# Performance work log

Measured on AMD Instinct MI355X. Metric: run time of the kernel, lower is better.

The kernel has to match this reference:

```python
import jax, jax.numpy as jnp
import numpy as np

N, L, D = 512, 40, 128      # batch, peptide length, embedding dim
O, K, MHC = 256, 9, 34      # out_channels, kernel_size, mhc_len
STRIDE = 1


def setup_inputs() -> dict:
    key = jax.random.key(0)
    k1, k2, k3 = jax.random.split(key, 3)
    peptide_x = jax.random.normal(k1, (N, L, D), dtype=jnp.float32)
    mhc_x = jax.random.normal(k2, (N, MHC, D), dtype=jnp.float32)
    weight = jax.random.normal(k3, (O, K, MHC), dtype=jnp.float32) * 0.02  # truncated_normal std=0.02 approx
    bias = jnp.zeros((O,), dtype=jnp.float32)
    return {"peptide_x": peptide_x, "mhc_x": mhc_x, "weight": weight, "bias": bias}


def reference(peptide_x, mhc_x, weight, bias):
    # Per-sample dynamic kernel generation: [n, O, d, K]
    kernel = jax.nn.relu(jnp.einsum('nld,okl->nodk', mhc_x, weight))
    k = weight.shape[1]
    T = (peptide_x.shape[1] - k) // STRIDE + 1  # conv1d output length
    # Sliding windows of the peptide: [n, T, K, d]
    idx = jnp.arange(T)[:, None] * STRIDE + jnp.arange(k)[None, :]
    win = peptide_x[:, idx, :]
    # Grouped (groups=batch) conv1d as a batched contraction: [n, O, T]
    out = jnp.einsum('ntkd,nodk->not', win, kernel) + bias[None, :, None]
    return out
```

## Files before the change

kernel.cpp:

```cpp
#include <hip/hip_runtime.h>
#include <hip/hip_bf16.h>

typedef unsigned short u16;
typedef unsigned int u32;
typedef __bf16 bf16x8 __attribute__((ext_vector_type(8)));
typedef float f32x4 __attribute__((ext_vector_type(4)));
typedef unsigned int u32x4 __attribute__((ext_vector_type(4)));
typedef unsigned int u32x2 __attribute__((ext_vector_type(2)));

#define NN 512
#define LL 40
#define DD 128
#define OO 256
#define KK 9
#define MHCL 34
#define TT 32
#define OC 32
#define OCPG 4
#define PSTR 136
#define MSTR 72
#define KSTR 136
#define LPAD 64
#define WPADL 64

#define PEPT_U16 (LL * PSTR)
#define KERN_U16 (32 * KSTR)

__device__ __forceinline__ u16 f2bf(float x) {
    unsigned int u = __builtin_bit_cast(unsigned int, x);
    u = (u + 0x7FFFu + ((u >> 16) & 1u)) >> 16;
    return (u16)u;
}
__device__ __forceinline__ u32 pk2(float a, float b) {
    __hip_bfloat162 h = __float22bfloat162_rn(make_float2(a, b));
    u32 r;
    __builtin_memcpy(&r, &h, 4);
    return r;
}
__device__ __forceinline__ bf16x8 lds_read8(const u16* p) {
    u32x4 r;
    __builtin_memcpy(&r, __builtin_assume_aligned(p, 16), 16);
    return __builtin_bit_cast(bf16x8, r);
}
__device__ __forceinline__ f32x4 mfma16(bf16x8 a, bf16x8 b, f32x4 c) {
    return __builtin_amdgcn_mfma_f32_16x16x32_bf16(a, b, c, 0, 0, 0);
}

__global__ void w_convert(const float* __restrict__ wgt, u32* __restrict__ wp) {
    int i = blockIdx.x * 256 + threadIdx.x;
    if (i >= OO * KK * (WPADL / 2)) return;
    int o = i / (KK * (WPADL / 2));
    int r = i - o * (KK * (WPADL / 2));
    int k = r >> 5;
    int lp = (r & 31) << 1;
    const float* src = wgt + ((size_t)o * KK + k) * MHCL;
    float a = (lp     < MHCL) ? src[lp]     : 0.f;
    float b = (lp + 1 < MHCL) ? src[lp + 1] : 0.f;
    wp[i] = pk2(a, b);
}

template<bool PRE>
__global__ __launch_bounds__(512, 4)
void iconv_kernel(const float* __restrict__ pept,
                  const float* __restrict__ mhc,
                  const float* __restrict__ wgt,
                  const u16* __restrict__ wp,
                  const float* __restrict__ bias,
                  float* __restrict__ out)
{
    __shared__ __align__(16) u16 s_mem[PEPT_U16 + 4 * KERN_U16];

    const int tid  = threadIdx.x;
    const int wave = tid >> 6;
    const int grp  = wave >> 2;
    const int wl   = wave & 3;
    const int lane = tid & 63;
    const int quad = lane >> 4;
    const int l16  = lane & 15;

    const int n = blockIdx.x;

    u16* const s_pept = s_mem;
    u16* const kb0    = s_mem + PEPT_U16 + grp * (2 * KERN_U16);

    auto loadW = [&](int o_base, int k, bf16x8 wF[2][2]) {
        if (PRE) {
            #pragma unroll
            for (int mt = 0; mt < 2; ++mt) {
                const u16* wr = wp + ((size_t)(o_base + mt * 16 + l16) * KK + k) * WPADL;
                u32x4 r0, r1;
                __builtin_memcpy(&r0, __builtin_assume_aligned(wr + quad * 8, 16), 16);
                __builtin_memcpy(&r1, __builtin_assume_aligned(wr + 32 + quad * 8, 16), 16);
                wF[mt][0] = __builtin_bit_cast(bf16x8, r0);
                wF[mt][1] = __builtin_bit_cast(bf16x8, r1);
            }
        } else {
            #pragma unroll
            for (int mt = 0; mt < 2; ++mt) {
                const float* wrow = wgt + ((size_t)(o_base + mt * 16 + l16) * KK + k) * MHCL;
                float w8[8];
                __builtin_memcpy(w8, __builtin_assume_aligned(wrow + quad * 8, 8), 32);
                u16 h0[8];
                #pragma unroll
                for (int j = 0; j < 8; ++j) h0[j] = f2bf(w8[j]);
                __builtin_memcpy(&wF[mt][0], h0, 16);
                u16 h1[8] = {0,0,0,0,0,0,0,0};
                if (quad == 0) { h1[0] = f2bf(wrow[32]); h1[1] = f2bf(wrow[33]); }
                __builtin_memcpy(&wF[mt][1], h1, 16);
            }
        }
    };

    bf16x8 wFh[2][2];
    loadW((grp * OCPG) * OC, 0, wFh);

    {
        const float* mg = mhc + (size_t)n * MHCL * DD;
        #pragma unroll 1
        for (int i = tid; i < DD * (LPAD / 8); i += 512) {
            int g = i >> 7, d = i & 127;
            u32x4 hh;
            #pragma unroll
            for (int jj = 0; jj < 4; ++jj) {
                int l = g * 8 + jj * 2;
                float a = (l     < MHCL) ? mg[(size_t)l * DD + d]       : 0.f;
                float b = (l + 1 < MHCL) ? mg[(size_t)(l + 1) * DD + d] : 0.f;
                hh[jj] = pk2(a, b);
            }
            __builtin_memcpy(__builtin_assume_aligned(&s_mem[d * MSTR + g * 8], 16), &hh, 16);
        }
    }
    __syncthreads();

    bf16x8 aF[2][2];
    #pragma unroll
    for (int ntl = 0; ntl < 2; ++ntl) {
        const int d = (wl * 2 + ntl) * 16 + l16;
        aF[ntl][0] = lds_read8(&s_mem[d * MSTR + quad * 8]);
        aF[ntl][1] = lds_read8(&s_mem[d * MSTR + 32 + quad * 8]);
    }
    __syncthreads();

    {
        const float* pg = pept + (size_t)n * LL * DD;
        #pragma unroll 1
        for (int i = tid; i < (LL * DD) / 4; i += 512) {
            int row = i >> 5, c4 = (i & 31) << 2;
            f32x4 v;
            __builtin_memcpy(&v, __builtin_assume_aligned(pg + row * DD + c4, 16), 16);
            u32x2 h = { pk2(v[0], v[1]), pk2(v[2], v[3]) };
            __builtin_memcpy(__builtin_assume_aligned(&s_pept[row * PSTR + c4], 8), &h, 8);
        }
    }
    __syncthreads();

    auto stage1 = [&](const bf16x8 wF[2][2], int buf) {
        u16* const kbw = kb0 + buf * KERN_U16;
        #pragma unroll
        for (int ntl = 0; ntl < 2; ++ntl) {
            const int nt = wl * 2 + ntl;
            f32x4 c0 = {0.f,0.f,0.f,0.f}, c1 = c0;
            #pragma unroll
            for (int ki = 0; ki < 2; ++ki) {
                c0 = mfma16(aF[ntl][ki], wF[0][ki], c0);
                c1 = mfma16(aF[ntl][ki], wF[1][ki], c1);
            }
            u32x2 p0 = { pk2(fmaxf(c0[0], 0.f), fmaxf(c0[1], 0.f)),
                         pk2(fmaxf(c0[2], 0.f), fmaxf(c0[3], 0.f)) };
            u32x2 p1 = { pk2(fmaxf(c1[0], 0.f), fmaxf(c1[1], 0.f)),
                         pk2(fmaxf(c1[2], 0.f), fmaxf(c1[3], 0.f)) };
            __builtin_memcpy(__builtin_assume_aligned(&kbw[l16 * KSTR + nt * 16 + quad * 4], 8), &p0, 8);
            __builtin_memcpy(__builtin_assume_aligned(&kbw[(16 + l16) * KSTR + nt * 16 + quad * 4], 8), &p1, 8);
        }
    };

    const int off = wl * 32 + quad * 8;

    #pragma unroll 1
    for (int oci = 0; oci < OCPG; ++oci) {
        const int o_base = (grp * OCPG + oci) * OC;
        f32x4 acc00 = {0.f,0.f,0.f,0.f}, acc01 = acc00, acc10 = acc00, acc11 = acc00;

        bf16x8 wCur[2][2];
        loadW(o_base, 1, wCur);
        stage1(wFh, 0);

        #pragma unroll
        for (int k = 0; k < KK; ++k) {
            const u16* kbr = kb0 + (k & 1) * KERN_U16;
            bf16x8 bk0 = lds_read8(&kbr[l16 * KSTR + off]);
            bf16x8 bk1 = lds_read8(&kbr[(16 + l16) * KSTR + off]);
            bf16x8 ap0 = lds_read8(&s_pept[(k + l16) * PSTR + off]);
            bf16x8 ap1 = lds_read8(&s_pept[(k + 16 + l16) * PSTR + off]);
            bf16x8 wNext[2][2];
            if (k + 2 <= KK - 1) loadW(o_base, k + 2, wNext);
            if (k + 1 <= KK - 1) stage1(wCur, (k + 1) & 1);
            acc00 = mfma16(ap0, bk0, acc00);
            acc01 = mfma16(ap0, bk1, acc01);
            acc10 = mfma16(ap1, bk0, acc10);
            acc11 = mfma16(ap1, bk1, acc11);
            if (k + 2 <= KK - 1) {
                #pragma unroll
                for (int a = 0; a < 2; ++a)
                    #pragma unroll
                    for (int b = 0; b < 2; ++b) wCur[a][b] = wNext[a][b];
            }
        }

        if (oci + 1 < OCPG) loadW((grp * OCPG + oci + 1) * OC, 0, wFh);

        __syncthreads();
        float* red = (float*)kb0;
        if (wl < 2) {
            float* rw = red + wl * (TT * 33);
            #pragma unroll
            for (int r = 0; r < 4; ++r) {
                rw[(quad * 4 + r) * 33 + l16]           = acc00[r];
                rw[(quad * 4 + r) * 33 + 16 + l16]      = acc01[r];
                rw[(16 + quad * 4 + r) * 33 + l16]      = acc10[r];
                rw[(16 + quad * 4 + r) * 33 + 16 + l16] = acc11[r];
            }
        }
        __syncthreads();
        if (wl >= 2) {
            float* rw = red + (wl - 2) * (TT * 33);
            #pragma unroll
            for (int r = 0; r < 4; ++r) {
                rw[(quad * 4 + r) * 33 + l16]           += acc00[r];
                rw[(quad * 4 + r) * 33 + 16 + l16]      += acc01[r];
                rw[(16 + quad * 4 + r) * 33 + l16]      += acc10[r];
                rw[(16 + quad * 4 + r) * 33 + 16 + l16] += acc11[r];
            }
        }
        __syncthreads();

        {
            const int lt = tid & 255;
            const int o  = lt >> 3;
            const int t0 = (lt & 7) * 4;
            const float bv = bias[o_base + o];
            f32x4 res;
            #pragma unroll
            for (int j = 0; j < 4; ++j) {
                int idx = (t0 + j) * 33 + o;
                res[j] = red[idx] + red[TT * 33 + idx] + bv;
            }
            float* op = out + ((size_t)n * OO + o_base + o) * TT + t0;
            __builtin_memcpy(__builtin_assume_aligned(op, 16), &res, 16);
        }
        __syncthreads();
    }
}

extern "C" void kernel_launch(void* const* d_in, const int* in_sizes, int n_in,
                              void* d_out, int out_size, void* d_ws, size_t ws_size,
                              hipStream_t stream) {
    const float* pept = (const float*)d_in[0];
    const float* mhc  = (const float*)d_in[1];
    const float* wgt  = (const float*)d_in[2];
    const float* bias = (const float*)d_in[3];
    float* out = (float*)d_out;

    const size_t w_bytes = (size_t)OO * KK * WPADL * sizeof(u16);
    if (ws_size >= w_bytes) {
        w_convert<<<dim3((OO * KK * (WPADL / 2) + 255) / 256), dim3(256), 0, stream>>>(wgt, (u32*)d_ws);
        iconv_kernel<true><<<dim3(NN), dim3(512), 0, stream>>>(pept, mhc, wgt, (const u16*)d_ws, bias, out);
    } else {
        iconv_kernel<false><<<dim3(NN), dim3(512), 0, stream>>>(pept, mhc, wgt, nullptr, bias, out);
    }
}
```

Measured before the change: 144.2 us.

## Process two output-channel chunks per pass, sharing peptide fragments and barriers

Each wave group now handles two 32-channel chunks (A and B) per outer iteration instead of one, so it makes 2 passes rather than 4. Within a pass, the peptide window fragments read from LDS are reused for both chunks' MFMAs. The two cross-wave reductions share one set of barriers, which halves the number of __syncthreads. In exchange, the previous double-buffered dynamic-kernel scheme with two-step weight prefetch is replaced by one-step-ahead weight loads and per-chunk LDS buffers. This raises register pressure and may expose more global weight-load latency.

```diff
diff --git a/kernel.cpp b/kernel.cpp
--- a/kernel.cpp
+++ b/kernel.cpp
@@ -16,7 +16,6 @@
 #define MHCL 34
 #define TT 32
 #define OC 32
-#define OCPG 4
 #define PSTR 136
 #define MSTR 72
 #define KSTR 136
@@ -81,7 +80,8 @@
     const int n = blockIdx.x;
 
     u16* const s_pept = s_mem;
-    u16* const kb0    = s_mem + PEPT_U16 + grp * (2 * KERN_U16);
+    u16* const kbA    = s_mem + PEPT_U16 + grp * (2 * KERN_U16);
+    u16* const kbB    = kbA + KERN_U16;
 
     auto loadW = [&](int o_base, int k, bf16x8 wF[2][2]) {
         if (PRE) {
@@ -111,8 +111,9 @@
         }
     };
 
-    bf16x8 wFh[2][2];
-    loadW((grp * OCPG) * OC, 0, wFh);
+    bf16x8 wA[2][2], wB[2][2];
+    loadW(grp * 128, 0, wA);
+    loadW(grp * 128 + OC, 0, wB);
 
     {
         const float* mg = mhc + (size_t)n * MHCL * DD;
@@ -154,8 +155,7 @@
     }
     __syncthreads();
 
-    auto stage1 = [&](const bf16x8 wF[2][2], int buf) {
-        u16* const kbw = kb0 + buf * KERN_U16;
+    auto stage1 = [&](const bf16x8 wF[2][2], u16* kbw) {
         #pragma unroll
         for (int ntl = 0; ntl < 2; ++ntl) {
             const int nt = wl * 2 + ntl;
@@ -177,76 +177,95 @@
     const int off = wl * 32 + quad * 8;
 
     #pragma unroll 1
-    for (int oci = 0; oci < OCPG; ++oci) {
-        const int o_base = (grp * OCPG + oci) * OC;
-        f32x4 acc00 = {0.f,0.f,0.f,0.f}, acc01 = acc00, acc10 = acc00, acc11 = acc00;
-
-        bf16x8 wCur[2][2];
-        loadW(o_base, 1, wCur);
-        stage1(wFh, 0);
+    for (int oci = 0; oci < 2; ++oci) {
+        const int o_baseA = grp * 128 + oci * 64;
+        const int o_baseB = o_baseA + OC;
+        f32x4 aA00 = {0.f,0.f,0.f,0.f}, aA01 = aA00, aA10 = aA00, aA11 = aA00;
+        f32x4 aB00 = aA00, aB01 = aA00, aB10 = aA00, aB11 = aA00;
 
         #pragma unroll
         for (int k = 0; k < KK; ++k) {
-            const u16* kbr = kb0 + (k & 1) * KERN_U16;
-            bf16x8 bk0 = lds_read8(&kbr[l16 * KSTR + off]);
-            bf16x8 bk1 = lds_read8(&kbr[(16 + l16) * KSTR + off]);
-            bf16x8 ap0 = lds_read8(&s_pept[(k + l16) * PSTR + off]);
-            bf16x8 ap1 = lds_read8(&s_pept[(k + 16 + l16) * PSTR + off]);
-            bf16x8 wNext[2][2];
-            if (k + 2 <= KK - 1) loadW(o_base, k + 2, wNext);
-            if (k + 1 <= KK - 1) stage1(wCur, (k + 1) & 1);
-            acc00 = mfma16(ap0, bk0, acc00);
-            acc01 = mfma16(ap0, bk1, acc01);
-            acc10 = mfma16(ap1, bk0, acc10);
-            acc11 = mfma16(ap1, bk1, acc11);
-            if (k + 2 <= KK - 1) {
+            stage1(wA, kbA);
+            stage1(wB, kbB);
+            if (k < KK - 1) {
+                loadW(o_baseA, k + 1, wA);
+                loadW(o_baseB, k + 1, wB);
+            }
+            bf16x8 ap0  = lds_read8(&s_pept[(k + l16) * PSTR + off]);
+            bf16x8 ap1  = lds_read8(&s_pept[(k + 16 + l16) * PSTR + off]);
+            bf16x8 bkA0 = lds_read8(&kbA[l16 * KSTR + off]);
+            bf16x8 bkA1 = lds_read8(&kbA[(16 + l16) * KSTR + off]);
+            aA00 = mfma16(ap0, bkA0, aA00);
+            aA01 = mfma16(ap0, bkA1, aA01);
+            aA10 = mfma16(ap1, bkA0, aA10);
+            aA11 = mfma16(ap1, bkA1, aA11);
+            bf16x8 bkB0 = lds_read8(&kbB[l16 * KSTR + off]);
+            bf16x8 bkB1 = lds_read8(&kbB[(16 + l16) * KSTR + off]);
+            aB00 = mfma16(ap0, bkB0, aB00);
+            aB01 = mfma16(ap0, bkB1, aB01);
+            aB10 = mfma16(ap1, bkB0, aB10);
+            aB11 = mfma16(ap1, bkB1, aB11);
+        }
+
+        if (oci == 0) {
+            loadW(grp * 128 + 64, 0, wA);
+            loadW(grp * 128 + 96, 0, wB);
+        }
+
+        __syncthreads();
+        float* redA = (float*)kbA;
+        float* redB = redA + 2 * TT * 33;
+        if (wl < 2) {
+            float* rwA = redA + wl * (TT * 33);
+            float* rwB = redB + wl * (TT * 33);
+            #pragma unroll
+            for (int r = 0; r < 4; ++r) {
+                rwA[(quad * 4 + r) * 33 + l16]           = aA00[r];
+                rwA[(quad * 4 + r) * 33 + 16 + l16]      = aA01[r];
+                rwA[(16 + quad * 4 + r) * 33 + l16]      = aA10[r];
+                rwA[(16 + quad * 4 + r) * 33 + 16 + l16] = aA11[r];
+                rwB[(quad * 4 + r) * 33 + l16]           = aB00[r];
+                rwB[(quad * 4 + r) * 33 + 16 + l16]      = aB01[r];
+                rwB[(16 + quad * 4 + r) * 33 + l16]      = aB10[r];
+                rwB[(16 + quad * 4 + r) * 33 + 16 + l16] = aB11[r];
+            }
+        }
+        __syncthreads();
+        if (wl >= 2) {
+            float* rwA = redA + (wl - 2) * (TT * 33);
+            float* rwB = redB + (wl - 2) * (TT * 33);
+            #pragma unroll
+            for (int r = 0; r < 4; ++r) {
+                rwA[(quad * 4 + r) * 33 + l16]           += aA00[r];
+                rwA[(quad * 4 + r) * 33 + 16 + l16]      += aA01[r];
+                rwA[(16 + quad * 4 + r) * 33 + l16]      += aA10[r];
+                rwA[(16 + quad * 4 + r) * 33 + 16 + l16] += aA11[r];
+                rwB[(quad * 4 + r) * 33 + l16]           += aB00[r];
+                rwB[(quad * 4 + r) * 33 + 16 + l16]      += aB01[r];
+                rwB[(16 + quad * 4 + r) * 33 + l16]      += aB10[r];
+                rwB[(16 + quad * 4 + r) * 33 + 16 + l16] += aB11[r];
+            }
+        }
+        __syncthreads();
+
+        {
+            const int lt  = tid & 255;
+            const int o   = lt >> 3;
+            const int t0  = (lt & 7) * 4;
+            #pragma unroll
+            for (int ocS = 0; ocS < 2; ++ocS) {
+                const float* rp = ocS ? redB : redA;
+                const int og  = (ocS ? o_baseB : o_baseA) + o;
+                const float bv = bias[og];
+                f32x4 res;
                 #pragma unroll
-                for (int a = 0; a < 2; ++a)
-                    #pragma unroll
-                    for (int b = 0; b < 2; ++b) wCur[a][b] = wNext[a][b];
-            }
-        }
-
-        if (oci + 1 < OCPG) loadW((grp * OCPG + oci + 1) * OC, 0, wFh);
-
-        __syncthreads();
-        float* red = (float*)kb0;
-        if (wl < 2) {
-            float* rw = red + wl * (TT * 33);
-            #pragma unroll
-            for (int r = 0; r < 4; ++r) {
-                rw[(quad * 4 + r) * 33 + l16]           = acc00[r];
-                rw[(quad * 4 + r) * 33 + 16 + l16]      = acc01[r];
-                rw[(16 + quad * 4 + r) * 33 + l16]      = acc10[r];
-                rw[(16 + quad * 4 + r) * 33 + 16 + l16] = acc11[r];
-            }
-        }
-        __syncthreads();
-        if (wl >= 2) {
-            float* rw = red + (wl - 2) * (TT * 33);
-            #pragma unroll
-            for (int r = 0; r < 4; ++r) {
-                rw[(quad * 4 + r) * 33 + l16]           += acc00[r];
-                rw[(quad * 4 + r) * 33 + 16 + l16]      += acc01[r];
-                rw[(16 + quad * 4 + r) * 33 + l16]      += acc10[r];
-                rw[(16 + quad * 4 + r) * 33 + 16 + l16] += acc11[r];
-            }
-        }
-        __syncthreads();
-
-        {
-            const int lt = tid & 255;
-            const int o  = lt >> 3;
-            const int t0 = (lt & 7) * 4;
-            const float bv = bias[o_base + o];
-            f32x4 res;
-            #pragma unroll
-            for (int j = 0; j < 4; ++j) {
-                int idx = (t0 + j) * 33 + o;
-                res[j] = red[idx] + red[TT * 33 + idx] + bv;
-            }
-            float* op = out + ((size_t)n * OO + o_base + o) * TT + t0;
-            __builtin_memcpy(__builtin_assume_aligned(op, 16), &res, 16);
+                for (int j = 0; j < 4; ++j) {
+                    int idx = (t0 + j) * 33 + o;
+                    res[j] = rp[idx] + rp[TT * 33 + idx] + bv;
+                }
+                float* op = out + ((size_t)n * OO + og) * TT + t0;
+                __builtin_memcpy(__builtin_assume_aligned(op, 16), &res, 16);
+            }
         }
         __syncthreads();
     }
```

After: 149.8 us. 1.04x slower.
